# Optimization experiments

Hardware: AMD Instinct MI355X
Metric: run time of the kernel (lower is better)

The kernel has to match this reference:

```python
import jax, jax.numpy as jnp
import numpy as np

B, W, H, C = 4, 32, 32, 128   # image feature map
S, D = 256, 512               # text seq len, text embed dim
NC = 64                       # num_channels (attention inner dim)


def setup_inputs() -> dict:
    key = jax.random.key(0)
    ks = jax.random.split(key, 16)
    def dense(k, din, dout):
        return jax.random.normal(k, (din, dout), jnp.float32) / np.sqrt(din)
    return {
        "x": jax.random.normal(ks[0], (B, W, H, C), jnp.float32),
        "s": jax.random.normal(ks[1], (B, S, D), jnp.float32),
        "a": jax.random.randint(ks[2], (B, S), 0, 2).astype(jnp.float32),
        "Wq": dense(ks[3], C, NC),  "bq": jnp.zeros((NC,), jnp.float32),
        "Wkx": dense(ks[4], C, NC), "bkx": jnp.zeros((NC,), jnp.float32),
        "Wvx": dense(ks[5], C, NC), "bvx": jnp.zeros((NC,), jnp.float32),
        "Wks": dense(ks[6], D, NC), "bks": jnp.zeros((NC,), jnp.float32),
        "Wvs": dense(ks[7], D, NC), "bvs": jnp.zeros((NC,), jnp.float32),
        "Wout": dense(ks[8], NC, C), "bout": jnp.zeros((C,), jnp.float32),
        "ln_scale": jnp.ones((C,), jnp.float32),
        "ln_bias": jnp.zeros((C,), jnp.float32),
    }


def reference(x, s, a, Wq, bq, Wkx, bkx, Wvx, bvx, Wks, bks, Wvs, bvs,
              Wout, bout, ln_scale, ln_bias):
    nc = Wq.shape[-1]
    # mask text embeddings: repeat(a,'b s -> b s d') * s
    te = s * a[:, :, None]
    # projections
    q = x @ Wq + bq            # (b,w,h,c)
    kx = x @ Wkx + bkx         # (b,w,h,c)
    vx = x @ Vx_dummy if False else x @ Wvx + bvx
    ks = te @ Wks + bks        # (b,s,c)
    vs = te @ Wvs + bvs        # (b,s,c)
    # broadcast-add spatial and text keys/values -> (b,w,h,s,c)
    k = kx[:, :, :, None, :] + ks[:, None, None, :, :]
    v = vx[:, :, :, None, :] + vs[:, None, None, :, :]
    # attention matrix over channels: v^T @ k contracted over s -> (b,w,h,c,c)
    attn = jnp.einsum('bwhsc,bwhsd->bwhcd', v, k) / jnp.sqrt(jnp.asarray(nc, x.dtype))
    attn = jax.nn.softmax(attn, axis=-1)
    # q applied through the channel-channel attention -> (b,w,h,c)
    out = jnp.einsum('bwhj,bwhjk->bwhk', q, attn)
    # output projection back to x channels, residual, layernorm
    out = out @ Wout + bout
    x = x + out
    mu = jnp.mean(x, axis=-1, keepdims=True)
    var = jnp.var(x, axis=-1, keepdims=True)
    x = (x - mu) * jax.lax.rsqrt(var + 1e-6) * ln_scale + ln_bias
    return x
```

## Files before the change

### kernel.cpp

```cpp
#include <hip/hip_runtime.h>
#include <hip/hip_bf16.h>

#define BB 4
#define SS 256
#define DD 512
#define CC 128
#define NC 64
#define PXB 4
#define NTEXT 128

struct XRole { float xl[8][CC]; };
struct TRole { float tel[8][DD];
               float part[2][2][8][NC];
               float ksl[8][NC]; float vsl[8][NC]; };
union ProjSH { XRole xr; TRole tr; };

__global__ __launch_bounds__(256) void proj_kernel(
    const float* __restrict__ x,
    const float* __restrict__ Wq,  const float* __restrict__ bq,
    const float* __restrict__ Wkx, const float* __restrict__ bkx,
    const float* __restrict__ Wvx, const float* __restrict__ bvx,
    const float* __restrict__ s,   const float* __restrict__ a,
    const float* __restrict__ Wks, const float* __restrict__ bks,
    const float* __restrict__ Wvs, const float* __restrict__ bvs,
    float* __restrict__ P, float* __restrict__ Mw,
    float* __restrict__ Ksw, float* __restrict__ Vsw)
{
    __shared__ ProjSH sh;
    const int t = threadIdx.x;
    const int w = t >> 6, lane = t & 63;
    const int blk = blockIdx.x;

    if (blk < NTEXT) {
        const int row0 = blk * 8;
        const int b = row0 >> 8;
        {
            const float4* s4 = (const float4*)(s + (size_t)row0 * DD);
            #pragma unroll
            for (int j = 0; j < 4; ++j) {
                const int i = t + j * 256;
                const int r = i >> 7;
                const float am = a[row0 + r];
                float4 v = s4[i];
                v.x *= am; v.y *= am; v.z *= am; v.w *= am;
                ((float4*)&sh.tr.tel[0][0])[i] = v;
            }
        }
        __syncthreads();

        const int m = w & 1, h = w >> 1;
        const int kb = h * 256;
        const int cg4 = (lane & 15) * 4;
        const int ksub = lane >> 4;
        const float* __restrict__ Wm = m ? Wvs : Wks;

        float4 acc[8] = {};
        #pragma unroll 2
        for (int j = 0; j < 64; ++j) {
            const int k = kb + 4 * j + ksub;
            const float4 wv = *(const float4*)(Wm + (size_t)k * NC + cg4);
            #pragma unroll
            for (int r = 0; r < 8; ++r) {
                const float tv = sh.tr.tel[r][k];
                acc[r].x = fmaf(tv, wv.x, acc[r].x);
                acc[r].y = fmaf(tv, wv.y, acc[r].y);
                acc[r].z = fmaf(tv, wv.z, acc[r].z);
                acc[r].w = fmaf(tv, wv.w, acc[r].w);
            }
        }
        #pragma unroll
        for (int r = 0; r < 8; ++r) {
            #pragma unroll
            for (int off = 16; off <= 32; off <<= 1) {
                acc[r].x += __shfl_down(acc[r].x, off);
                acc[r].y += __shfl_down(acc[r].y, off);
                acc[r].z += __shfl_down(acc[r].z, off);
                acc[r].w += __shfl_down(acc[r].w, off);
            }
        }
        if (lane < 16) {
            #pragma unroll
            for (int r = 0; r < 8; ++r)
                *(float4*)&sh.tr.part[m][h][r][cg4] = acc[r];
        }
        __syncthreads();

        #pragma unroll
        for (int i = t; i < 1024; i += 256) {
            const int mm = i >> 9;
            const int r = (i >> 6) & 7;
            const int col = i & 63;
            const float v = sh.tr.part[mm][0][r][col] + sh.tr.part[mm][1][r][col]
                          + (mm ? bvs[col] : bks[col]);
            if (mm) sh.tr.vsl[r][col] = v; else sh.tr.ksl[r][col] = v;
        }
        __syncthreads();

        if (w == 0) {
            float sk = 0.f;
            #pragma unroll
            for (int r = 0; r < 8; ++r) sk += sh.tr.ksl[r][lane];
            atomicAdd(&Ksw[b * NC + lane], sk);
        } else if (w == 1) {
            float sv = 0.f;
            #pragma unroll
            for (int r = 0; r < 8; ++r) sv += sh.tr.vsl[r][lane];
            atomicAdd(&Vsw[b * NC + lane], sv);
        }

        float* __restrict__ Mb = Mw + (size_t)b * NC * NC;
        #pragma unroll 4
        for (int j = 0; j < 16; ++j) {
            const int idx = t + j * 256;
            const int c = idx >> 6;
            float pm = 0.f;
            #pragma unroll
            for (int r = 0; r < 8; ++r)
                pm = fmaf(sh.tr.vsl[r][c], sh.tr.ksl[r][lane], pm);
            atomicAdd(Mb + idx, pm);
        }
    } else {
        const int px0 = (blk - NTEXT) * 8;
        ((float4*)&sh.xr.xl[0][0])[t] =
            ((const float4*)(x + (size_t)px0 * CC))[t];
        __syncthreads();
        if (w < 3) {
            const float* __restrict__ Wm = (w == 0) ? Wq : (w == 1 ? Wkx : Wvx);
            const float* __restrict__ bm = (w == 0) ? bq : (w == 1 ? bkx : bvx);
            const int ksub = lane >> 4;
            const int cg4 = (lane & 15) * 4;
            float4 acc[8] = {};
            #pragma unroll 4
            for (int j = 0; j < 32; ++j) {
                const int k = 4 * j + ksub;
                const float4 wv = *(const float4*)(Wm + (size_t)k * NC + cg4);
                #pragma unroll
                for (int px = 0; px < 8; ++px) {
                    const float xv = sh.xr.xl[px][k];
                    acc[px].x = fmaf(xv, wv.x, acc[px].x);
                    acc[px].y = fmaf(xv, wv.y, acc[px].y);
                    acc[px].z = fmaf(xv, wv.z, acc[px].z);
                    acc[px].w = fmaf(xv, wv.w, acc[px].w);
                }
            }
            #pragma unroll
            for (int px = 0; px < 8; ++px) {
                #pragma unroll
                for (int off = 16; off <= 32; off <<= 1) {
                    acc[px].x += __shfl_down(acc[px].x, off);
                    acc[px].y += __shfl_down(acc[px].y, off);
                    acc[px].z += __shfl_down(acc[px].z, off);
                    acc[px].w += __shfl_down(acc[px].w, off);
                }
            }
            if (ksub == 0) {
                const float4 bb = *(const float4*)(bm + cg4);
                #pragma unroll
                for (int px = 0; px < 8; ++px) {
                    float4 v;
                    v.x = acc[px].x + bb.x; v.y = acc[px].y + bb.y;
                    v.z = acc[px].z + bb.z; v.w = acc[px].w + bb.w;
                    *(float4*)(P + (size_t)(px0 + px) * 192 + w * 64 + cg4) = v;
                }
            }
        }
    }
}

__global__ __launch_bounds__(256) void pixel_kernel(
    const float* __restrict__ x, const float* __restrict__ P,
    const float* __restrict__ Wout, const float* __restrict__ bout,
    const float* __restrict__ ln_scale, const float* __restrict__ ln_bias,
    const float* __restrict__ Mw, const float* __restrict__ Ksw,
    const float* __restrict__ Vsw,
    float* __restrict__ out)
{
    __shared__ float Ml[NC * 65];
    __shared__ float projl[PXB][192];
    __shared__ float xl[PXB][CC];
    __shared__ float rsl[PXB][NC];
    __shared__ float mxl[PXB][NC];
    __shared__ float outl[PXB][NC];
    __shared__ float Ksl[NC], Vsl[NC];
    __shared__ float redl[2][2][4];

    const int t = threadIdx.x;
    const int w = t >> 6, lane = t & 63;
    const int px0g = blockIdx.x * PXB;
    const int b = px0g >> 10;

    {
        const float4* P4 = (const float4*)(P + (size_t)px0g * 192);
        for (int i = t; i < PXB * 192 / 4; i += 256)
            ((float4*)&projl[0][0])[i] = P4[i];
        const float4* x4 = (const float4*)(x + (size_t)px0g * CC);
        for (int i = t; i < PXB * CC / 4; i += 256)
            ((float4*)&xl[0][0])[i] = x4[i];
        const float* Mb = Mw + (size_t)b * NC * NC;
        for (int i = t; i < NC * NC; i += 256)
            Ml[(i >> 6) * 65 + (i & 63)] = Mb[i];
        if (t < NC) { Ksl[t] = Ksw[b * NC + t]; Vsl[t] = Vsw[b * NC + t]; }
    }
    __syncthreads();

    {
        const int px = w, c = lane;
        const float vxc = projl[px][128 + c];
        const float qc  = projl[px][c];
        const float uc  = fmaf(256.0f, vxc, Vsl[c]);
        float mx = -3.4e38f;
        #pragma unroll
        for (int d = 0; d < NC; ++d) {
            const float A = fmaf(uc, projl[px][64 + d],
                                 fmaf(vxc, Ksl[d], Ml[c * 65 + d])) * 0.125f;
            mx = fmaxf(mx, A);
        }
        float sum = 0.f;
        #pragma unroll
        for (int d = 0; d < NC; ++d) {
            const float A = fmaf(uc, projl[px][64 + d],
                                 fmaf(vxc, Ksl[d], Ml[c * 65 + d])) * 0.125f;
            sum += __expf(A - mx);
        }
        rsl[px][c] = qc / sum;
        mxl[px][c] = mx;
    }
    __syncthreads();

    {
        const int px = w, d = lane;
        const float kxd = projl[px][64 + d];
        const float Ksd = Ksl[d];
        float acc = 0.f;
        #pragma unroll 4
        for (int c = 0; c < NC; ++c) {
            const float vxc = projl[px][128 + c];
            const float uc = fmaf(256.0f, vxc, Vsl[c]);
            const float A = fmaf(uc, kxd, fmaf(vxc, Ksd, Ml[c * 65 + d])) * 0.125f;
            acc = fmaf(rsl[px][c], __expf(A - mxl[px][c]), acc);
        }
        outl[px][d] = acc;
    }
    __syncthreads();

    {
        const int col = t & 127;
        const int pxg = t >> 7;
        const int px0 = 2 * pxg, px1 = px0 + 1;
        float acc0 = 0.f, acc1 = 0.f;
        #pragma unroll 4
        for (int k = 0; k < NC; ++k) {
            const float wv = Wout[k * CC + col];
            acc0 = fmaf(outl[px0][k], wv, acc0);
            acc1 = fmaf(outl[px1][k], wv, acc1);
        }
        const float bb = bout[col];
        const float y0 = acc0 + bb + xl[px0][col];
        const float y1 = acc1 + bb + xl[px1][col];

        float s10 = y0, s20 = y0 * y0, s11 = y1, s21 = y1 * y1;
        #pragma unroll
        for (int off = 32; off >= 1; off >>= 1) {
            s10 += __shfl_down(s10, off);
            s20 += __shfl_down(s20, off);
            s11 += __shfl_down(s11, off);
            s21 += __shfl_down(s21, off);
        }
        const int half = (t >> 6) & 1;
        if (lane == 0) {
            redl[pxg][half][0] = s10; redl[pxg][half][1] = s20;
            redl[pxg][half][2] = s11; redl[pxg][half][3] = s21;
        }
        __syncthreads();
        const float S10 = redl[pxg][0][0] + redl[pxg][1][0];
        const float S20 = redl[pxg][0][1] + redl[pxg][1][1];
        const float S11 = redl[pxg][0][2] + redl[pxg][1][2];
        const float S21 = redl[pxg][0][3] + redl[pxg][1][3];
        const float mu0 = S10 * (1.f / 128.f);
        const float var0 = S20 * (1.f / 128.f) - mu0 * mu0;
        const float mu1 = S11 * (1.f / 128.f);
        const float var1 = S21 * (1.f / 128.f) - mu1 * mu1;
        const float r0 = rsqrtf(var0 + 1e-6f), r1 = rsqrtf(var1 + 1e-6f);
        const float gg = ln_scale[col], be = ln_bias[col];
        out[(size_t)(px0g + px0) * CC + col] = (y0 - mu0) * r0 * gg + be;
        out[(size_t)(px0g + px1) * CC + col] = (y1 - mu1) * r1 * gg + be;
    }
}

extern "C" void kernel_launch(void* const* d_in, const int* in_sizes, int n_in,
                              void* d_out, int out_size, void* d_ws, size_t ws_size,
                              hipStream_t stream) {
    const float* x        = (const float*)d_in[0];
    const float* s        = (const float*)d_in[1];
    const float* a        = (const float*)d_in[2];
    const float* Wq       = (const float*)d_in[3];
    const float* bq       = (const float*)d_in[4];
    const float* Wkx      = (const float*)d_in[5];
    const float* bkx      = (const float*)d_in[6];
    const float* Wvx      = (const float*)d_in[7];
    const float* bvx      = (const float*)d_in[8];
    const float* Wks      = (const float*)d_in[9];
    const float* bks      = (const float*)d_in[10];
    const float* Wvs      = (const float*)d_in[11];
    const float* bvs      = (const float*)d_in[12];
    const float* Wout     = (const float*)d_in[13];
    const float* bout     = (const float*)d_in[14];
    const float* ln_scale = (const float*)d_in[15];
    const float* ln_bias  = (const float*)d_in[16];

    float* ws  = (float*)d_ws;
    float* Mw  = ws;
    float* Ksw = ws + 16384;
    float* Vsw = ws + 16640;
    float* Pw  = ws + 16896;

    hipMemsetAsync(Mw, 0, 16896 * sizeof(float), stream);

    proj_kernel<<<NTEXT + 512, 256, 0, stream>>>(
        x, Wq, bq, Wkx, bkx, Wvx, bvx, s, a, Wks, bks, Wvs, bvs,
        Pw, Mw, Ksw, Vsw);
    pixel_kernel<<<(BB * 1024) / PXB, 256, 0, stream>>>(
        x, Pw, Wout, bout, ln_scale, ln_bias, Mw, Ksw, Vsw, (float*)d_out);
}
```

Before: 119.4 us.

## Fuse projection and pixel kernels into one persistent kernel with grid barrier

Merges the projection kernel and the per-pixel attention/layernorm kernel into a single launch of 1024 blocks, separated by a software grid barrier built on an atomic counter. The barrier counter is zeroed by the existing memset. This is meant to remove the second kernel launch and the gap between the two kernels. In exchange it depends on all 1024 blocks being co-resident (launch bounds ask for 4 blocks per CU), adds spin-wait cost, and uses a union shared-memory layout.

New measurement: 377.7 us. 216% more time.

```diff
diff --git a/kernel.cpp b/kernel.cpp
--- a/kernel.cpp
+++ b/kernel.cpp
@@ -8,14 +8,29 @@
 #define NC 64
 #define PXB 4
 #define NTEXT 128
+#define NGRID 1024
 
 struct XRole { float xl[8][CC]; };
 struct TRole { float tel[8][DD];
                float part[2][2][8][NC];
                float ksl[8][NC]; float vsl[8][NC]; };
-union ProjSH { XRole xr; TRole tr; };
-
-__global__ __launch_bounds__(256) void proj_kernel(
+struct PixSH { float Ml[NC * 65]; float projl[PXB][192]; float xl[PXB][CC];
+               float rsl[PXB][NC]; float mxl[PXB][NC]; float outl[PXB][NC];
+               float Ksl[NC]; float Vsl[NC]; float redl[2][2][4]; };
+union MegaSH { XRole xr; TRole tr; PixSH p3; };
+
+__device__ __forceinline__ void grid_barrier(unsigned* cnt) {
+    __syncthreads();
+    if (threadIdx.x == 0) {
+        __threadfence();
+        __hip_atomic_fetch_add(cnt, 1u, __ATOMIC_ACQ_REL, __HIP_MEMORY_SCOPE_AGENT);
+        while (__hip_atomic_load(cnt, __ATOMIC_ACQUIRE, __HIP_MEMORY_SCOPE_AGENT) < NGRID)
+            __builtin_amdgcn_s_sleep(8);
+    }
+    __syncthreads();
+}
+
+__global__ __launch_bounds__(256, 4) void mega_kernel(
     const float* __restrict__ x,
     const float* __restrict__ Wq,  const float* __restrict__ bq,
     const float* __restrict__ Wkx, const float* __restrict__ bkx,
@@ -23,10 +38,14 @@
     const float* __restrict__ s,   const float* __restrict__ a,
     const float* __restrict__ Wks, const float* __restrict__ bks,
     const float* __restrict__ Wvs, const float* __restrict__ bvs,
+    const float* __restrict__ Wout, const float* __restrict__ bout,
+    const float* __restrict__ ln_scale, const float* __restrict__ ln_bias,
     float* __restrict__ P, float* __restrict__ Mw,
-    float* __restrict__ Ksw, float* __restrict__ Vsw)
+    float* __restrict__ Ksw, float* __restrict__ Vsw,
+    unsigned* __restrict__ bar,
+    float* __restrict__ out)
 {
-    __shared__ ProjSH sh;
+    __shared__ MegaSH sh;
     const int t = threadIdx.x;
     const int w = t >> 6, lane = t & 63;
     const int blk = blockIdx.x;
@@ -119,7 +138,7 @@
                 pm = fmaf(sh.tr.vsl[r][c], sh.tr.ksl[r][lane], pm);
             atomicAdd(Mb + idx, pm);
         }
-    } else {
+    } else if (blk < NTEXT + 512) {
         const int px0 = (blk - NTEXT) * 8;
         ((float4*)&sh.xr.xl[0][0])[t] =
             ((const float4*)(x + (size_t)px0 * CC))[t];
@@ -165,125 +184,112 @@
             }
         }
     }
-}
-
-__global__ __launch_bounds__(256) void pixel_kernel(
-    const float* __restrict__ x, const float* __restrict__ P,
-    const float* __restrict__ Wout, const float* __restrict__ bout,
-    const float* __restrict__ ln_scale, const float* __restrict__ ln_bias,
-    const float* __restrict__ Mw, const float* __restrict__ Ksw,
-    const float* __restrict__ Vsw,
-    float* __restrict__ out)
-{
-    __shared__ float Ml[NC * 65];
-    __shared__ float projl[PXB][192];
-    __shared__ float xl[PXB][CC];
-    __shared__ float rsl[PXB][NC];
-    __shared__ float mxl[PXB][NC];
-    __shared__ float outl[PXB][NC];
-    __shared__ float Ksl[NC], Vsl[NC];
-    __shared__ float redl[2][2][4];
-
-    const int t = threadIdx.x;
-    const int w = t >> 6, lane = t & 63;
-    const int px0g = blockIdx.x * PXB;
-    const int b = px0g >> 10;
+
+    grid_barrier(bar);
 
     {
-        const float4* P4 = (const float4*)(P + (size_t)px0g * 192);
-        for (int i = t; i < PXB * 192 / 4; i += 256)
-            ((float4*)&projl[0][0])[i] = P4[i];
-        const float4* x4 = (const float4*)(x + (size_t)px0g * CC);
-        for (int i = t; i < PXB * CC / 4; i += 256)
-            ((float4*)&xl[0][0])[i] = x4[i];
-        const float* Mb = Mw + (size_t)b * NC * NC;
-        for (int i = t; i < NC * NC; i += 256)
-            Ml[(i >> 6) * 65 + (i & 63)] = Mb[i];
-        if (t < NC) { Ksl[t] = Ksw[b * NC + t]; Vsl[t] = Vsw[b * NC + t]; }
-    }
-    __syncthreads();
-
-    {
-        const int px = w, c = lane;
-        const float vxc = projl[px][128 + c];
-        const float qc  = projl[px][c];
-        const float uc  = fmaf(256.0f, vxc, Vsl[c]);
-        float mx = -3.4e38f;
-        #pragma unroll
-        for (int d = 0; d < NC; ++d) {
-            const float A = fmaf(uc, projl[px][64 + d],
-                                 fmaf(vxc, Ksl[d], Ml[c * 65 + d])) * 0.125f;
-            mx = fmaxf(mx, A);
-        }
-        float sum = 0.f;
-        #pragma unroll
-        for (int d = 0; d < NC; ++d) {
-            const float A = fmaf(uc, projl[px][64 + d],
-                                 fmaf(vxc, Ksl[d], Ml[c * 65 + d])) * 0.125f;
-            sum += __expf(A - mx);
-        }
-        rsl[px][c] = qc / sum;
-        mxl[px][c] = mx;
-    }
-    __syncthreads();
-
-    {
-        const int px = w, d = lane;
-        const float kxd = projl[px][64 + d];
-        const float Ksd = Ksl[d];
-        float acc = 0.f;
-        #pragma unroll 4
-        for (int c = 0; c < NC; ++c) {
-            const float vxc = projl[px][128 + c];
-            const float uc = fmaf(256.0f, vxc, Vsl[c]);
-            const float A = fmaf(uc, kxd, fmaf(vxc, Ksd, Ml[c * 65 + d])) * 0.125f;
-            acc = fmaf(rsl[px][c], __expf(A - mxl[px][c]), acc);
-        }
-        outl[px][d] = acc;
-    }
-    __syncthreads();
-
-    {
-        const int col = t & 127;
-        const int pxg = t >> 7;
-        const int px0 = 2 * pxg, px1 = px0 + 1;
-        float acc0 = 0.f, acc1 = 0.f;
-        #pragma unroll 4
-        for (int k = 0; k < NC; ++k) {
-            const float wv = Wout[k * CC + col];
-            acc0 = fmaf(outl[px0][k], wv, acc0);
-            acc1 = fmaf(outl[px1][k], wv, acc1);
-        }
-        const float bb = bout[col];
-        const float y0 = acc0 + bb + xl[px0][col];
-        const float y1 = acc1 + bb + xl[px1][col];
-
-        float s10 = y0, s20 = y0 * y0, s11 = y1, s21 = y1 * y1;
-        #pragma unroll
-        for (int off = 32; off >= 1; off >>= 1) {
-            s10 += __shfl_down(s10, off);
-            s20 += __shfl_down(s20, off);
-            s11 += __shfl_down(s11, off);
-            s21 += __shfl_down(s21, off);
-        }
-        const int half = (t >> 6) & 1;
-        if (lane == 0) {
-            redl[pxg][half][0] = s10; redl[pxg][half][1] = s20;
-            redl[pxg][half][2] = s11; redl[pxg][half][3] = s21;
-        }
-        __syncthreads();
-        const float S10 = redl[pxg][0][0] + redl[pxg][1][0];
-        const float S20 = redl[pxg][0][1] + redl[pxg][1][1];
-        const float S11 = redl[pxg][0][2] + redl[pxg][1][2];
-        const float S21 = redl[pxg][0][3] + redl[pxg][1][3];
-        const float mu0 = S10 * (1.f / 128.f);
-        const float var0 = S20 * (1.f / 128.f) - mu0 * mu0;
-        const float mu1 = S11 * (1.f / 128.f);
-        const float var1 = S21 * (1.f / 128.f) - mu1 * mu1;
-        const float r0 = rsqrtf(var0 + 1e-6f), r1 = rsqrtf(var1 + 1e-6f);
-        const float gg = ln_scale[col], be = ln_bias[col];
-        out[(size_t)(px0g + px0) * CC + col] = (y0 - mu0) * r0 * gg + be;
-        out[(size_t)(px0g + px1) * CC + col] = (y1 - mu1) * r1 * gg + be;
+        const int px0g = blk * PXB;
+        const int b = px0g >> 10;
+
+        {
+            const float4* P4 = (const float4*)(P + (size_t)px0g * 192);
+            for (int i = t; i < PXB * 192 / 4; i += 256)
+                ((float4*)&sh.p3.projl[0][0])[i] = P4[i];
+            const float4* x4 = (const float4*)(x + (size_t)px0g * CC);
+            for (int i = t; i < PXB * CC / 4; i += 256)
+                ((float4*)&sh.p3.xl[0][0])[i] = x4[i];
+            const float* Mb = Mw + (size_t)b * NC * NC;
+            for (int i = t; i < NC * NC; i += 256)
+                sh.p3.Ml[(i >> 6) * 65 + (i & 63)] = Mb[i];
+            if (t < NC) {
+                sh.p3.Ksl[t] = Ksw[b * NC + t];
+                sh.p3.Vsl[t] = Vsw[b * NC + t];
+            }
+        }
+        __syncthreads();
+
+        {
+            const int px = w, c = lane;
+            const float vxc = sh.p3.projl[px][128 + c];
+            const float qc  = sh.p3.projl[px][c];
+            const float uc  = fmaf(256.0f, vxc, sh.p3.Vsl[c]);
+            float mx = -3.4e38f;
+            #pragma unroll
+            for (int d = 0; d < NC; ++d) {
+                const float A = fmaf(uc, sh.p3.projl[px][64 + d],
+                                     fmaf(vxc, sh.p3.Ksl[d], sh.p3.Ml[c * 65 + d])) * 0.125f;
+                mx = fmaxf(mx, A);
+            }
+            float sum = 0.f;
+            #pragma unroll
+            for (int d = 0; d < NC; ++d) {
+                const float A = fmaf(uc, sh.p3.projl[px][64 + d],
+                                     fmaf(vxc, sh.p3.Ksl[d], sh.p3.Ml[c * 65 + d])) * 0.125f;
+                sum += __expf(A - mx);
+            }
+            sh.p3.rsl[px][c] = qc / sum;
+            sh.p3.mxl[px][c] = mx;
+        }
+        __syncthreads();
+
+        {
+            const int px = w, d = lane;
+            const float kxd = sh.p3.projl[px][64 + d];
+            const float Ksd = sh.p3.Ksl[d];
+            float acc = 0.f;
+            #pragma unroll 4
+            for (int c = 0; c < NC; ++c) {
+                const float vxc = sh.p3.projl[px][128 + c];
+                const float uc = fmaf(256.0f, vxc, sh.p3.Vsl[c]);
+                const float A = fmaf(uc, kxd, fmaf(vxc, Ksd, sh.p3.Ml[c * 65 + d])) * 0.125f;
+                acc = fmaf(sh.p3.rsl[px][c], __expf(A - sh.p3.mxl[px][c]), acc);
+            }
+            sh.p3.outl[px][d] = acc;
+        }
+        __syncthreads();
+
+        {
+            const int col = t & 127;
+            const int pxg = t >> 7;
+            const int px0 = 2 * pxg, px1 = px0 + 1;
+            float acc0 = 0.f, acc1 = 0.f;
+            #pragma unroll 4
+            for (int k = 0; k < NC; ++k) {
+                const float wv = Wout[k * CC + col];
+                acc0 = fmaf(sh.p3.outl[px0][k], wv, acc0);
+                acc1 = fmaf(sh.p3.outl[px1][k], wv, acc1);
+            }
+            const float bb = bout[col];
+            const float y0 = acc0 + bb + sh.p3.xl[px0][col];
+            const float y1 = acc1 + bb + sh.p3.xl[px1][col];
+
+            float s10 = y0, s20 = y0 * y0, s11 = y1, s21 = y1 * y1;
+            #pragma unroll
+            for (int off = 32; off >= 1; off >>= 1) {
+                s10 += __shfl_down(s10, off);
+                s20 += __shfl_down(s20, off);
+                s11 += __shfl_down(s11, off);
+                s21 += __shfl_down(s21, off);
+            }
+            const int half = (t >> 6) & 1;
+            if (lane == 0) {
+                sh.p3.redl[pxg][half][0] = s10; sh.p3.redl[pxg][half][1] = s20;
+                sh.p3.redl[pxg][half][2] = s11; sh.p3.redl[pxg][half][3] = s21;
+            }
+            __syncthreads();
+            const float S10 = sh.p3.redl[pxg][0][0] + sh.p3.redl[pxg][1][0];
+            const float S20 = sh.p3.redl[pxg][0][1] + sh.p3.redl[pxg][1][1];
+            const float S11 = sh.p3.redl[pxg][0][2] + sh.p3.redl[pxg][1][2];
+            const float S21 = sh.p3.redl[pxg][0][3] + sh.p3.redl[pxg][1][3];
+            const float mu0 = S10 * (1.f / 128.f);
+            const float var0 = S20 * (1.f / 128.f) - mu0 * mu0;
+            const float mu1 = S11 * (1.f / 128.f);
+            const float var1 = S21 * (1.f / 128.f) - mu1 * mu1;
+            const float r0 = rsqrtf(var0 + 1e-6f), r1 = rsqrtf(var1 + 1e-6f);
+            const float gg = ln_scale[col], be = ln_bias[col];
+            out[(size_t)(px0g + px0) * CC + col] = (y0 - mu0) * r0 * gg + be;
+            out[(size_t)(px0g + px1) * CC + col] = (y1 - mu1) * r1 * gg + be;
+        }
     }
 }
 
@@ -312,13 +318,14 @@
     float* Mw  = ws;
     float* Ksw = ws + 16384;
     float* Vsw = ws + 16640;
-    float* Pw  = ws + 16896;
-
-    hipMemsetAsync(Mw, 0, 16896 * sizeof(float), stream);
-
-    proj_kernel<<<NTEXT + 512, 256, 0, stream>>>(
+    unsigned* bar = (unsigned*)(ws + 16896);
+    float* Pw  = ws + 17152;
+    float* outp = (float*)d_out;
+
+    hipMemsetAsync(Mw, 0, 17152 * sizeof(float), stream);
+
+    mega_kernel<<<NGRID, 256, 0, stream>>>(
         x, Wq, bq, Wkx, bkx, Wvx, bvx, s, a, Wks, bks, Wvs, bvs,
-        Pw, Mw, Ksw, Vsw);
-    pixel_kernel<<<(BB * 1024) / PXB, 256, 0, stream>>>(
-        x, Pw, Wout, bout, ln_scale, ln_bias, Mw, Ksw, Vsw, (float*)d_out);
+        Wout, bout, ln_scale, ln_bias,
+        Pw, Mw, Ksw, Vsw, bar, outp);
 }
```
